# Kernel tuning notes

Hardware: AMD Instinct MI355X
Metric: run time of the kernel (lower is better)

The kernel has to match this reference:

```python
import jax, jax.numpy as jnp
import numpy as np

NUM_PARTITIONS = 128
C = 32
D = 128
B, S, K = 4, 2048, 2


def setup_inputs() -> dict:
    key = jax.random.key(0)
    k1, k2, k3, k4 = jax.random.split(key, 4)
    partition_indices = jax.random.randint(k1, (B, S, K), 0, NUM_PARTITIONS)
    keys = jax.random.normal(k2, (B, S, K, C), dtype=jnp.float32)
    values = jax.random.normal(k3, (B, S, D), dtype=jnp.float32)
    queries = jax.random.normal(k4, (B, S, D), dtype=jnp.float32)
    return {
        "partition_indices": partition_indices,
        "keys": keys,
        "values": values,
        "queries": queries,
    }


def reference(partition_indices, keys, values, queries):
    # States start at zero; update() scatter-adds outer(k_bti, v_bt) into
    # states[p_bti]. read() then computes sum_i states[p_bti].mean(axis=0) * q_bt.
    b, s, k, c = keys.shape
    d = values.shape[-1]
    # outer products: [B,S,K,c,d]
    outer = keys[..., :, None] * values[:, :, None, None, :]
    flat_outer = outer.reshape(b * s * k, c, d)
    seg = partition_indices.reshape(-1)
    # scatter-add into partitioned states [P, c, d]
    states = jax.ops.segment_sum(flat_outer, seg, num_segments=NUM_PARTITIONS)
    means = states.mean(axis=1)  # [P, d]
    gathered = means[partition_indices]  # [B, S, K, d]
    out = gathered.sum(axis=2) * queries  # [B, S, d]
    return out
```

## Files before the change

kernel.cpp:

```cpp
#include <hip/hip_runtime.h>
#include <hip/hip_bf16.h>

#define P_  128
#define C_  32
#define D_  128
#define BS_ 8192
#define PD_ (P_*D_)
#define NB_ 256

__global__ __launch_bounds__(512) void scatter_partials(
    const int* __restrict__ idx, const float* __restrict__ keys,
    const float* __restrict__ values, float* __restrict__ partials)
{
    __shared__ float lmeans[PD_];
    float4* lm4 = (float4*)lmeans;
    const int tid = threadIdx.x;
    for (int i = tid; i < PD_ / 4; i += 512) lm4[i] = float4{0.f, 0.f, 0.f, 0.f};
    __syncthreads();

    const int lane = tid & 63;
    const int wave = tid >> 6;
    const int rbase = blockIdx.x * 32 + wave;

    float kv[4], va[4], vb[4];
    int2  ii[4];
    #pragma unroll
    for (int j = 0; j < 4; ++j) {
        const int r = rbase + 8 * j;
        kv[j] = keys[(size_t)r * 64 + lane];
        ii[j] = ((const int2*)idx)[r];
        va[j] = values[(size_t)r * D_ + lane];
        vb[j] = values[(size_t)r * D_ + 64 + lane];
    }

    #pragma unroll
    for (int j = 0; j < 4; ++j) {
        float s = kv[j];
        s += __shfl_xor(s, 16);
        s += __shfl_xor(s, 8);
        s += __shfl_xor(s, 4);
        s += __shfl_xor(s, 2);
        s += __shfl_xor(s, 1);
        const float ks0 = __shfl(s, 0)  * (1.f / 32.f);
        const float ks1 = __shfl(s, 32) * (1.f / 32.f);
        atomicAdd(&lmeans[ii[j].x * D_ + lane],      ks0 * va[j]);
        atomicAdd(&lmeans[ii[j].x * D_ + 64 + lane], ks0 * vb[j]);
        atomicAdd(&lmeans[ii[j].y * D_ + lane],      ks1 * va[j]);
        atomicAdd(&lmeans[ii[j].y * D_ + 64 + lane], ks1 * vb[j]);
    }
    __syncthreads();

    float4* dst = (float4*)(partials + (size_t)blockIdx.x * PD_);
    for (int i = tid; i < PD_ / 4; i += 512) dst[i] = lm4[i];
}

__global__ __launch_bounds__(256) void reduce_partials(
    const float* __restrict__ partials, float* __restrict__ means)
{
    __shared__ float red[4][64];
    const int t  = threadIdx.x;
    const int el = t & 63;
    const int g  = t >> 6;
    const int e  = blockIdx.x * 64 + el;
    float s = 0.f;
    #pragma unroll 8
    for (int j = 0; j < 64; ++j)
        s += partials[(size_t)(g * 64 + j) * PD_ + e];
    red[g][el] = s;
    __syncthreads();
    if (t < 64)
        means[blockIdx.x * 64 + t] = red[0][t] + red[1][t] + red[2][t] + red[3][t];
}

__global__ __launch_bounds__(256) void emit_out(
    const int* __restrict__ idx, const float* __restrict__ means,
    const float* __restrict__ queries, float* __restrict__ out)
{
    const int gid = blockIdx.x * 256 + threadIdx.x;
    const int row = gid >> 5;
    const int d4  = gid & 31;
    const int2 ii = ((const int2*)idx)[row];
    const float4 q = ((const float4*)queries)[gid];
    const float4* m4 = (const float4*)means;
    const float4 a = m4[ii.x * 32 + d4];
    const float4 b = m4[ii.y * 32 + d4];
    float4 o;
    o.x = (a.x + b.x) * q.x;
    o.y = (a.y + b.y) * q.y;
    o.z = (a.z + b.z) * q.z;
    o.w = (a.w + b.w) * q.w;
    ((float4*)out)[gid] = o;
}

extern "C" void kernel_launch(void* const* d_in, const int* in_sizes, int n_in,
                              void* d_out, int out_size, void* d_ws, size_t ws_size,
                              hipStream_t stream) {
    const int*   idx     = (const int*)d_in[0];
    const float* keys    = (const float*)d_in[1];
    const float* values  = (const float*)d_in[2];
    const float* queries = (const float*)d_in[3];
    float* out = (float*)d_out;
    float* ws  = (float*)d_ws;

    float* partials = ws;
    float* means    = ws + (size_t)NB_ * PD_;

    scatter_partials<<<NB_, 512, 0, stream>>>(idx, keys, values, partials);
    reduce_partials<<<PD_ / 64, 256, 0, stream>>>(partials, means);
    emit_out<<<(BS_ * D_ / 4) / 256, 256, 0, stream>>>(idx, means, queries, out);
}
```

Measured before the change: 88.63 us.

## Fuse scatter, reduce and emit into one cooperative kernel with grid syncs

Merges the three kernel launches into a single cooperative kernel of 256 blocks that uses grid-wide syncs between the scatter, partial-reduction and output phases. This removes two kernel launch gaps and their dependency bubbles. In exchange, the reduce and emit phases now run on only 256 blocks of 512 threads instead of wider grids. Each block is large, using 64KB of shared memory, so cooperative launch depends on all 256 blocks being co-resident.

```diff
diff --git a/kernel.cpp b/kernel.cpp
--- a/kernel.cpp
+++ b/kernel.cpp
@@ -1,5 +1,7 @@
 #include <hip/hip_runtime.h>
-#include <hip/hip_bf16.h>
+#include <hip/hip_cooperative_groups.h>
+
+namespace cg = cooperative_groups;
 
 #define P_  128
 #define C_  32
@@ -8,13 +10,16 @@
 #define PD_ (P_*D_)
 #define NB_ 256
 
-__global__ __launch_bounds__(512) void scatter_partials(
+__global__ __launch_bounds__(512) void fused_all(
     const int* __restrict__ idx, const float* __restrict__ keys,
-    const float* __restrict__ values, float* __restrict__ partials)
+    const float* __restrict__ values, const float* __restrict__ queries,
+    float* __restrict__ partials, float* __restrict__ means,
+    float* __restrict__ out)
 {
     __shared__ float lmeans[PD_];
     float4* lm4 = (float4*)lmeans;
     const int tid = threadIdx.x;
+
     for (int i = tid; i < PD_ / 4; i += 512) lm4[i] = float4{0.f, 0.f, 0.f, 0.f};
     __syncthreads();
 
@@ -50,46 +55,52 @@
     }
     __syncthreads();
 
-    float4* dst = (float4*)(partials + (size_t)blockIdx.x * PD_);
-    for (int i = tid; i < PD_ / 4; i += 512) dst[i] = lm4[i];
-}
+    {
+        float4* dst = (float4*)(partials + (size_t)blockIdx.x * PD_);
+        for (int i = tid; i < PD_ / 4; i += 512) dst[i] = lm4[i];
+    }
 
-__global__ __launch_bounds__(256) void reduce_partials(
-    const float* __restrict__ partials, float* __restrict__ means)
-{
-    __shared__ float red[4][64];
-    const int t  = threadIdx.x;
-    const int el = t & 63;
-    const int g  = t >> 6;
+    __threadfence();
+    cg::this_grid().sync();
+
+    const int el = tid & 63;
+    const int g  = tid >> 6;
     const int e  = blockIdx.x * 64 + el;
-    float s = 0.f;
+    float s2 = 0.f;
     #pragma unroll 8
-    for (int j = 0; j < 64; ++j)
-        s += partials[(size_t)(g * 64 + j) * PD_ + e];
-    red[g][el] = s;
+    for (int j = 0; j < 32; ++j)
+        s2 += partials[(size_t)(g * 32 + j) * PD_ + e];
+    lmeans[g * 64 + el] = s2;
     __syncthreads();
-    if (t < 64)
-        means[blockIdx.x * 64 + t] = red[0][t] + red[1][t] + red[2][t] + red[3][t];
-}
+    if (tid < 64) {
+        float m = lmeans[tid];
+        #pragma unroll
+        for (int g2 = 1; g2 < 8; ++g2) m += lmeans[g2 * 64 + tid];
+        means[blockIdx.x * 64 + tid] = m;
+    }
 
-__global__ __launch_bounds__(256) void emit_out(
-    const int* __restrict__ idx, const float* __restrict__ means,
-    const float* __restrict__ queries, float* __restrict__ out)
-{
-    const int gid = blockIdx.x * 256 + threadIdx.x;
-    const int row = gid >> 5;
-    const int d4  = gid & 31;
-    const int2 ii = ((const int2*)idx)[row];
-    const float4 q = ((const float4*)queries)[gid];
+    __threadfence();
+    cg::this_grid().sync();
+
     const float4* m4 = (const float4*)means;
-    const float4 a = m4[ii.x * 32 + d4];
-    const float4 b = m4[ii.y * 32 + d4];
-    float4 o;
-    o.x = (a.x + b.x) * q.x;
-    o.y = (a.y + b.y) * q.y;
-    o.z = (a.z + b.z) * q.z;
-    o.w = (a.w + b.w) * q.w;
-    ((float4*)out)[gid] = o;
+    const float4* q4 = (const float4*)queries;
+    float4*       o4 = (float4*)out;
+    #pragma unroll
+    for (int it = 0; it < 2; ++it) {
+        const int gid = blockIdx.x * 1024 + it * 512 + tid;
+        const int row = gid >> 5;
+        const int d4  = gid & 31;
+        const int2 p  = ((const int2*)idx)[row];
+        const float4 q = q4[gid];
+        const float4 a = m4[p.x * 32 + d4];
+        const float4 b = m4[p.y * 32 + d4];
+        float4 o;
+        o.x = (a.x + b.x) * q.x;
+        o.y = (a.y + b.y) * q.y;
+        o.z = (a.z + b.z) * q.z;
+        o.w = (a.w + b.w) * q.w;
+        o4[gid] = o;
+    }
 }
 
 extern "C" void kernel_launch(void* const* d_in, const int* in_sizes, int n_in,
@@ -105,7 +116,8 @@
     float* partials = ws;
     float* means    = ws + (size_t)NB_ * PD_;
 
-    scatter_partials<<<NB_, 512, 0, stream>>>(idx, keys, values, partials);
-    reduce_partials<<<PD_ / 64, 256, 0, stream>>>(partials, means);
-    emit_out<<<(BS_ * D_ / 4) / 256, 256, 0, stream>>>(idx, means, queries, out);
+    void* args[] = {(void*)&idx, (void*)&keys, (void*)&values, (void*)&queries,
+                    (void*)&partials, (void*)&means, (void*)&out};
+    hipLaunchCooperativeKernel((void*)fused_all, dim3(NB_), dim3(512),
+                               args, 0, stream);
 }
```

Measured after the change: 235.8 us. 166% more time.
